# Kernel tuning notes

Measured on AMD Instinct MI355X. Metric: run time of the kernel, lower is better.

The kernel has to match this reference:

```python
import jax, jax.numpy as jnp
import numpy as np

DIM = 48
D_STATE = 16
D_CONV = 4
EXPAND = 2
D_INNER = DIM * EXPAND          # 96
DT_RANK = (DIM + 15) // 16      # 3
EPS = 1e-5


def _interp2x_align_corners(x, axis):
    """Linear 2x upsample along one axis with align_corners=True."""
    n = x.shape[axis]
    out = 2 * n
    pos = jnp.arange(out, dtype=jnp.float32) * (n - 1) / (out - 1)
    lo = jnp.floor(pos).astype(jnp.int32)
    hi = jnp.minimum(lo + 1, n - 1)
    w = (pos - lo.astype(jnp.float32)).astype(x.dtype)
    shape = [1] * x.ndim
    shape[axis] = out
    w = w.reshape(shape)
    return jnp.take(x, lo, axis=axis) * (1 - w) + jnp.take(x, hi, axis=axis) * w


def _upsample_trilinear2x(x):
    for axis in (2, 3, 4):
        x = _interp2x_align_corners(x, axis)
    return x


def _conv3d(x, w, b, pad):
    y = jax.lax.conv_general_dilated(
        x, w, window_strides=(1, 1, 1), padding=[(pad, pad)] * 3,
        dimension_numbers=('NCDHW', 'OIDHW', 'NCDHW'))
    return y + b[None, :, None, None, None]


def _instance_norm(x):
    m = x.mean(axis=(2, 3, 4), keepdims=True)
    v = x.var(axis=(2, 3, 4), keepdims=True)  # biased var, as PyTorch InstanceNorm3d
    return (x - m) / jnp.sqrt(v + EPS)


def _mamba(u, in_proj_w, conv1d_w, conv1d_b, x_proj_w, dt_proj_w, dt_proj_b,
           A_log, D_param, out_proj_w):
    # u: (B, L, d_model)
    Bsz, L, _ = u.shape
    xz = jnp.einsum('bld,ed->ble', u, in_proj_w)        # (B, L, 2*Di)
    xi, z = jnp.split(xz, 2, axis=-1)                   # each (B, L, Di)
    # depthwise causal conv1d (pad left d_conv-1, crop to L == mamba's slice)
    xpad = jnp.pad(xi.transpose(0, 2, 1), ((0, 0), (0, 0), (D_CONV - 1, 0)))
    xc = jax.lax.conv_general_dilated(
        xpad, conv1d_w, window_strides=(1,), padding=[(0, 0)],
        dimension_numbers=('NCH', 'OIH', 'NCH'), feature_group_count=D_INNER)
    xs = jax.nn.silu((xc + conv1d_b[None, :, None]).transpose(0, 2, 1))  # (B, L, Di)

    dbc = jnp.einsum('bld,ed->ble', xs, x_proj_w)       # (B, L, dt_rank+2*N)
    dt, Bm, Cm = jnp.split(dbc, [DT_RANK, DT_RANK + D_STATE], axis=-1)
    delta = jax.nn.softplus(jnp.einsum('blr,dr->bld', dt, dt_proj_w) + dt_proj_b)

    A = -jnp.exp(A_log)                                  # (Di, N)
    dA = jnp.exp(jnp.einsum('bld,dn->bldn', delta, A))   # (B, L, Di, N)
    dBx = jnp.einsum('bld,bln->bldn', delta * xs, Bm)    # (B, L, Di, N)

    def step(h, inp):
        dA_t, dBx_t, C_t = inp                           # (B,Di,N),(B,Di,N),(B,N)
        h = dA_t * h + dBx_t
        y = jnp.einsum('bdn,bn->bd', h, C_t)
        return h, y

    h0 = jnp.zeros((Bsz, D_INNER, D_STATE), xs.dtype)
    _, ys = jax.lax.scan(step, h0,
                         (dA.transpose(1, 0, 2, 3), dBx.transpose(1, 0, 2, 3),
                          Cm.transpose(1, 0, 2)))
    y = ys.transpose(1, 0, 2) + D_param[None, None, :] * xs
    y = y * jax.nn.silu(z)
    return jnp.einsum('bld,ed->ble', y, out_proj_w)      # (B, L, d_model)


def setup_inputs() -> dict:
    key = jax.random.key(0)
    ks = jax.random.split(key, 16)
    s = 0.05
    f32 = jnp.float32
    inp = {
        'x': jax.random.normal(ks[0], (2, DIM, 12, 12, 12), f32),
        'Hx': jax.random.normal(ks[1], (2, DIM * 2, 24, 24, 24), f32),
        'W1': jax.random.normal(ks[2], (DIM, DIM * 3, 1, 1, 1), f32) * s,
        'b1': jax.random.normal(ks[3], (DIM,), f32) * s,
        'W2': jax.random.normal(ks[4], (DIM, DIM, 3, 3, 3), f32) * s,
        'b2': jax.random.normal(ks[5], (DIM,), f32) * s,
        'W3': jax.random.normal(ks[6], (DIM, DIM, 1, 1, 1), f32) * s,
        'b3': jax.random.normal(ks[7], (DIM,), f32) * s,
        'in_proj_w': jax.random.normal(ks[8], (2 * D_INNER, DIM), f32) * s,
        'conv1d_w': jax.random.normal(ks[9], (D_INNER, 1, D_CONV), f32) * s,
        'conv1d_b': jax.random.normal(ks[10], (D_INNER,), f32) * s,
        'x_proj_w': jax.random.normal(ks[11], (DT_RANK + 2 * D_STATE, D_INNER), f32) * s,
        'dt_proj_w': jax.random.normal(ks[12], (D_INNER, DT_RANK), f32) * s,
        'dt_proj_b': jax.random.normal(ks[13], (D_INNER,), f32) * 0.1,
        'A_log': jnp.log(jnp.tile(jnp.arange(1, D_STATE + 1, dtype=f32)[None, :],
                                  (D_INNER, 1))),
        'D_param': jnp.ones((D_INNER,), f32),
        'out_proj_w': jax.random.normal(ks[14], (DIM, D_INNER), f32) * s,
    }
    return inp


def reference(x, Hx, W1, b1, W2, b2, W3, b3, in_proj_w, conv1d_w, conv1d_b,
              x_proj_w, dt_proj_w, dt_proj_b, A_log, D_param, out_proj_w):
    up = _upsample_trilinear2x(x)                         # (B, dim, 2H, 2W, 2T)
    h = jnp.concatenate([up, Hx], axis=1)                 # (B, 3*dim, ...)
    h = _conv3d(h, W1, b1, 0)
    h = _conv3d(h, W2, b2, 1)
    h = _conv3d(h, W3, b3, 0)
    Lx = jax.nn.selu(_instance_norm(h))
    B, C, H, W, T = Lx.shape
    u = Lx.reshape(B, C, H * W * T).transpose(0, 2, 1)    # (B, L, C)
    ym = _mamba(u, in_proj_w, conv1d_w, conv1d_b, x_proj_w, dt_proj_w,
                dt_proj_b, A_log, D_param, out_proj_w)
    out = ym.transpose(0, 2, 1).reshape(B, C, H, W, T) + Lx
    return out
```

## Files before the change

### kernel.cpp

```cpp
#include <hip/hip_runtime.h>
#include <math.h>

#define NB 2
#define NCH 48
#define P 13824
#define DI 96
#define NSTATE 16
#define L 13824
#define CHUNK 128
#define NCK 108
#define TL 64

__device__ __forceinline__ float siluf(float x) { return x / (1.f + __expf(-x)); }
__device__ __forceinline__ float softplusf(float x) {
    return x > 0.f ? x + log1pf(expf(-x)) : log1pf(expf(x));
}

__global__ __launch_bounds__(256) void k_wtrans(const float* __restrict__ W2,
    const float* __restrict__ W1, const float* __restrict__ W3,
    const float* __restrict__ Wop, float* __restrict__ Wt, float* __restrict__ W1t,
    float* __restrict__ W3t, float* __restrict__ Wopt)
{
    int i = blockIdx.x * 256 + threadIdx.x;
    if (i < 62208) {
        int o = i / (48 * 27); int r = i % (48 * 27); int c = r / 27; int tap = r % 27;
        int og = o / 12, oi = o % 12;
        Wt[(((og * 27 + tap) * 48 + c) * 12) + oi] = W2[i];
    } else if (i < 62208 + 6912) {
        int j = i - 62208; int o = j / 144, c = j % 144;
        W1t[c * 48 + o] = W1[j];
    } else if (i < 62208 + 6912 + 2304) {
        int j = i - 62208 - 6912; int o = j / 48, c = j % 48;
        W3t[c * 48 + o] = W3[j];
    } else if (i < 62208 + 6912 + 2304 + 4608) {
        int j = i - 62208 - 6912 - 2304; int o = j / 96, q = j % 96;
        Wopt[q * 48 + o] = Wop[j];
    }
}

__global__ __launch_bounds__(128) void k_conv1(const float* __restrict__ x,
    const float* __restrict__ Hx, const float* __restrict__ W1t,
    const float* __restrict__ b1, float* __restrict__ h1)
{
    int t = blockIdx.x * 128 + threadIdx.x;
    int oh = blockIdx.y * 24;
    int b = t / P, p = t % P;
    int zi = p / 576, yi = (p / 24) % 24, xi_ = p % 24;
    float fpos; int z0, z1, y0, y1, x0, x1; float wz, wy, wx;
    fpos = (float)(zi * 11) / 23.0f; z0 = (int)floorf(fpos); wz = fpos - z0; z1 = min(z0 + 1, 11);
    fpos = (float)(yi * 11) / 23.0f; y0 = (int)floorf(fpos); wy = fpos - y0; y1 = min(y0 + 1, 11);
    fpos = (float)(xi_ * 11) / 23.0f; x0 = (int)floorf(fpos); wx = fpos - x0; x1 = min(x0 + 1, 11);
    int o000 = (z0*12+y0)*12+x0, o001 = (z0*12+y0)*12+x1;
    int o010 = (z0*12+y1)*12+x0, o011 = (z0*12+y1)*12+x1;
    int o100 = (z1*12+y0)*12+x0, o101 = (z1*12+y0)*12+x1;
    int o110 = (z1*12+y1)*12+x0, o111 = (z1*12+y1)*12+x1;
    float uz = 1.f - wz, uy = 1.f - wy, ux = 1.f - wx;
    float w000 = uz*uy*ux, w001 = uz*uy*wx, w010 = uz*wy*ux, w011 = uz*wy*wx;
    float w100 = wz*uy*ux, w101 = wz*uy*wx, w110 = wz*wy*ux, w111 = wz*wy*wx;

    float acc[24];
#pragma unroll
    for (int o = 0; o < 24; ++o) acc[o] = b1[oh + o];
    const float* xb = x + (size_t)b * 48 * 1728;
    for (int c0 = 0; c0 < 48; c0 += 4) {
        float a[4][8];
#pragma unroll
        for (int j = 0; j < 4; ++j) {
            const float* xc = xb + (c0 + j) * 1728;
            a[j][0] = xc[o000]; a[j][1] = xc[o001]; a[j][2] = xc[o010]; a[j][3] = xc[o011];
            a[j][4] = xc[o100]; a[j][5] = xc[o101]; a[j][6] = xc[o110]; a[j][7] = xc[o111];
        }
#pragma unroll
        for (int j = 0; j < 4; ++j) {
            float v = a[j][0]*w000 + a[j][1]*w001 + a[j][2]*w010 + a[j][3]*w011
                    + a[j][4]*w100 + a[j][5]*w101 + a[j][6]*w110 + a[j][7]*w111;
            const float* wr = W1t + (c0 + j) * 48 + oh;
#pragma unroll
            for (int o = 0; o < 24; ++o) acc[o] = fmaf(wr[o], v, acc[o]);
        }
    }
    const float* hb = Hx + (size_t)b * 96 * P + p;
    for (int c0 = 0; c0 < 96; c0 += 8) {
        float v[8];
#pragma unroll
        for (int j = 0; j < 8; ++j) v[j] = hb[(size_t)(c0 + j) * P];
#pragma unroll
        for (int j = 0; j < 8; ++j) {
            const float* wr = W1t + (48 + c0 + j) * 48 + oh;
#pragma unroll
            for (int o = 0; o < 24; ++o) acc[o] = fmaf(wr[o], v[j], acc[o]);
        }
    }
    float* out = h1 + (size_t)b * 48 * P + p;
#pragma unroll
    for (int o = 0; o < 24; ++o) out[(size_t)(oh+o) * P] = acc[o];
}

__global__ __launch_bounds__(512) void k_conv23(const float* __restrict__ h1,
    const float* __restrict__ Wt, const float* __restrict__ b2,
    const float* __restrict__ W3t, const float* __restrict__ b3,
    float* __restrict__ h3)
{
    __shared__ float tile[216 * 52];
    int blk = blockIdx.x;
    int b = blk / 216; int r = blk % 216;
    int tz = r / 36, ty = (r / 6) % 6, tx = r % 6;
    int z0 = tz*4 - 1, y0 = ty*4 - 1, x0 = tx*4 - 1;
    for (int i = threadIdx.x; i < 48 * 216; i += 512) {
        int c = i / 216; int q = i % 216;
        int lz = q / 36, ly = (q / 6) % 6, lx = q % 6;
        int gz = z0 + lz, gy = y0 + ly, gx = x0 + lx;
        float v = 0.f;
        if ((unsigned)gz < 24u && (unsigned)gy < 24u && (unsigned)gx < 24u)
            v = h1[((size_t)(b*48 + c)) * P + (gz*24 + gy)*24 + gx];
        tile[q*52 + c] = v;
    }
    __syncthreads();
    int lp = threadIdx.x & 63;
    int w  = __builtin_amdgcn_readfirstlane((int)(threadIdx.x >> 6));
    int og = w & 3, cc = w >> 2;
    int lz = lp >> 4, ly = (lp >> 2) & 3, lx = lp & 3;
    float acc[12];
#pragma unroll
    for (int i = 0; i < 12; ++i) acc[i] = cc ? 0.f : b2[og*12 + i];
#pragma unroll
    for (int dz = 0; dz < 3; ++dz)
#pragma unroll
    for (int dy = 0; dy < 3; ++dy)
#pragma unroll
    for (int dx = 0; dx < 3; ++dx) {
        int pos = (lz+dz)*36 + (ly+dy)*6 + (lx+dx);
        const float* tp = tile + pos*52 + cc*24;
        int tap = (dz*3 + dy)*3 + dx;
        const float* wt = Wt + (((size_t)og*27 + tap)*48 + cc*24)*12;
#pragma unroll
        for (int cq = 0; cq < 6; ++cq) {
            float4 v4 = *(const float4*)(tp + cq*4);
            const float* wq = wt + cq*48;
#pragma unroll
            for (int i = 0; i < 12; ++i) {
                acc[i] = fmaf(wq[i],      v4.x, acc[i]);
                acc[i] = fmaf(wq[12 + i], v4.y, acc[i]);
                acc[i] = fmaf(wq[24 + i], v4.z, acc[i]);
                acc[i] = fmaf(wq[36 + i], v4.w, acc[i]);
            }
        }
    }
    __syncthreads();
    if (cc == 1) {
        float* ex = tile + og * 768;
#pragma unroll
        for (int i = 0; i < 12; ++i) ex[i*64 + lp] = acc[i];
    }
    __syncthreads();
    if (cc == 0) {
        const float* ex = tile + og * 768;
        float* ht = tile + 3072;
#pragma unroll
        for (int i = 0; i < 12; ++i)
            ht[(og*12 + i)*64 + lp] = acc[i] + ex[i*64 + lp];
    }
    __syncthreads();
    const float* ht = tile + 3072;
    int oc0 = w * 6;
    float acc3[6];
#pragma unroll
    for (int j = 0; j < 6; ++j) acc3[j] = b3[oc0 + j];
    for (int c = 0; c < 48; ++c) {
        float v = ht[c*64 + lp];
        const float* wr = W3t + c*48 + oc0;
#pragma unroll
        for (int j = 0; j < 6; ++j) acc3[j] = fmaf(wr[j], v, acc3[j]);
    }
    int gz = tz*4 + lz, gy = ty*4 + ly, gx = tx*4 + lx;
    size_t pp = (size_t)(gz*24 + gy)*24 + gx;
#pragma unroll
    for (int j = 0; j < 6; ++j)
        h3[((size_t)(b*48) + oc0 + j) * P + pp] = acc3[j];
}

__global__ __launch_bounds__(256) void k_instnorm(float* __restrict__ h3)
{
    int bc = blockIdx.x;
    float4* src = (float4*)(h3 + (size_t)bc * P);
    float s = 0.f, s2 = 0.f;
    for (int i = threadIdx.x; i < 3456; i += 256) {
        float4 v = src[i];
        s  += v.x + v.y + v.z + v.w;
        s2 += v.x*v.x + v.y*v.y + v.z*v.z + v.w*v.w;
    }
    __shared__ float rs[4], rs2[4], mv[2];
    for (int off = 32; off; off >>= 1) { s += __shfl_down(s, off); s2 += __shfl_down(s2, off); }
    int wid = threadIdx.x >> 6;
    if ((threadIdx.x & 63) == 0) { rs[wid] = s; rs2[wid] = s2; }
    __syncthreads();
    if (threadIdx.x == 0) {
        s = rs[0] + rs[1] + rs[2] + rs[3];
        s2 = rs2[0] + rs2[1] + rs2[2] + rs2[3];
        float m = s / (float)P;
        float var = s2 / (float)P - m * m;
        mv[0] = m; mv[1] = rsqrtf(var + 1e-5f);
    }
    __syncthreads();
    float m = mv[0], istd = mv[1];
    const float kS = 1.0507009873554805f, kA = 1.6732632423543772f;
    for (int i = threadIdx.x; i < 3456; i += 256) {
        float4 v = src[i];
        float a0 = (v.x - m) * istd, a1 = (v.y - m) * istd;
        float a2 = (v.z - m) * istd, a3 = (v.w - m) * istd;
        v.x = a0 > 0.f ? kS * a0 : kS * kA * expm1f(a0);
        v.y = a1 > 0.f ? kS * a1 : kS * kA * expm1f(a1);
        v.z = a2 > 0.f ? kS * a2 : kS * kA * expm1f(a2);
        v.w = a3 > 0.f ? kS * a3 : kS * kA * expm1f(a3);
        src[i] = v;
    }
}

__global__ __launch_bounds__(192) void k_inproj(const float* __restrict__ Lx,
    const float* __restrict__ Wip, float* __restrict__ xi, float* __restrict__ z)
{
    int b = blockIdx.x / 432; int l0 = (blockIdx.x % 432) * 32;
    int e = threadIdx.x;
    float w[48];
#pragma unroll
    for (int c = 0; c < 48; ++c) w[c] = Wip[e*48 + c];
    float acc[32];
#pragma unroll
    for (int ll = 0; ll < 32; ++ll) acc[ll] = 0.f;
    const float* ub = Lx + (size_t)b * 48 * P + l0;
#pragma unroll 2
    for (int c = 0; c < 48; ++c) {
        const float* ur = ub + (size_t)c * P;
#pragma unroll
        for (int ll = 0; ll < 32; ++ll) acc[ll] = fmaf(w[c], ur[ll], acc[ll]);
    }
    float* dst = (e < 96) ? (xi + ((size_t)b * L + l0) * 96 + e)
                          : (z  + ((size_t)b * L + l0) * 96 + (e - 96));
#pragma unroll
    for (int ll = 0; ll < 32; ++ll) dst[(size_t)ll * 96] = acc[ll];
}

__global__ __launch_bounds__(256) void k_fxproj(const float* __restrict__ xi,
    const float* __restrict__ cw, const float* __restrict__ cb,
    const float* __restrict__ Wxp, const float* __restrict__ Wdt,
    const float* __restrict__ bdt, float* __restrict__ xs,
    float* __restrict__ delta, float* __restrict__ Bm, float* __restrict__ Cm)
{
    __shared__ float xs_t[TL][100];
    __shared__ float wx_t[35][100];
    __shared__ float wd_t[96][4];
    __shared__ float dt_t[TL][4];
    int blk = blockIdx.x;
    int b = blk / 216; int l0 = (blk % 216) * TL;
    int tid = threadIdx.x;

    for (int i = tid; i < 35 * 96; i += 256) wx_t[i / 96][i % 96] = Wxp[i];
    for (int i = tid; i < 96 * 3; i += 256) wd_t[i / 3][i % 3] = Wdt[i];
    for (int i = tid; i < 96; i += 256) wd_t[i][3] = bdt[i];

    int row = tid >> 2;
    int d0 = (tid & 3) * 24;
    int l = l0 + row;
    size_t t_glob = (size_t)b * L + l;
    const float* xib = xi + (size_t)b * L * 96;
    float* xsg = xs + t_glob * 96 + d0;
    int ls0 = l - 3;
#pragma unroll
    for (int jq = 0; jq < 6; ++jq) {
        int d = d0 + jq * 4;
        float4 t0 = *(const float4*)(cw + 4 * (d + 0));
        float4 t1 = *(const float4*)(cw + 4 * (d + 1));
        float4 t2 = *(const float4*)(cw + 4 * (d + 2));
        float4 t3 = *(const float4*)(cw + 4 * (d + 3));
        float4 acc = *(const float4*)(cb + d);
        float4 q0 = {0.f,0.f,0.f,0.f}, q1 = q0, q2 = q0;
        if (ls0 + 0 >= 0) q0 = *(const float4*)(xib + (size_t)(ls0 + 0) * 96 + d);
        if (ls0 + 1 >= 0) q1 = *(const float4*)(xib + (size_t)(ls0 + 1) * 96 + d);
        if (ls0 + 2 >= 0) q2 = *(const float4*)(xib + (size_t)(ls0 + 2) * 96 + d);
        float4 q3 = *(const float4*)(xib + (size_t)(ls0 + 3) * 96 + d);
        acc.x += t0.x*q0.x + t0.y*q1.x + t0.z*q2.x + t0.w*q3.x;
        acc.y += t1.x*q0.y + t1.y*q1.y + t1.z*q2.y + t1.w*q3.y;
        acc.z += t2.x*q0.z + t2.y*q1.z + t2.z*q2.z + t2.w*q3.z;
        acc.w += t3.x*q0.w + t3.y*q1.w + t3.z*q2.w + t3.w*q3.w;
        acc.x = siluf(acc.x); acc.y = siluf(acc.y);
        acc.z = siluf(acc.z); acc.w = siluf(acc.w);
        *(float4*)(&xs_t[row][d0 + jq * 4]) = acc;
        *(float4*)(xsg + jq * 4) = acc;
    }
    __syncthreads();

    int cq = tid & 3;
    float acc9[9];
#pragma unroll
    for (int k = 0; k < 9; ++k) acc9[k] = 0.f;
    const float* xrow = &xs_t[row][0];
#pragma unroll 4
    for (int j = 0; j < 24; ++j) {
        float4 xv = *(const float4*)(xrow + 4 * j);
#pragma unroll
        for (int k = 0; k < 9; ++k) {
            if (k < 8 || cq < 3) {
                int e = cq + 4 * k;
                float4 wv = *(const float4*)(&wx_t[e][4 * j]);
                acc9[k] = fmaf(wv.x, xv.x, fmaf(wv.y, xv.y,
                          fmaf(wv.z, xv.z, fmaf(wv.w, xv.w, acc9[k]))));
            }
        }
    }
#pragma unroll
    for (int k = 0; k < 9; ++k) {
        if (k < 8 || cq < 3) {
            int e = cq + 4 * k;
            if (e < 3)       dt_t[row][e] = acc9[k];
            else if (e < 19) Bm[t_glob * 16 + (e - 3)]  = acc9[k];
            else             Cm[t_glob * 16 + (e - 19)] = acc9[k];
        }
    }
    __syncthreads();

    float dt0 = dt_t[row][0], dt1 = dt_t[row][1], dt2 = dt_t[row][2];
    float* dl = delta + t_glob * 96 + d0;
#pragma unroll
    for (int jq = 0; jq < 6; ++jq) {
        float4 o;
        {
            float4 wv = *(const float4*)(&wd_t[d0 + jq*4 + 0][0]);
            o.x = softplusf(fmaf(wv.x, dt0, fmaf(wv.y, dt1, fmaf(wv.z, dt2, wv.w))));
        }
        {
            float4 wv = *(const float4*)(&wd_t[d0 + jq*4 + 1][0]);
            o.y = softplusf(fmaf(wv.x, dt0, fmaf(wv.y, dt1, fmaf(wv.z, dt2, wv.w))));
        }
        {
            float4 wv = *(const float4*)(&wd_t[d0 + jq*4 + 2][0]);
            o.z = softplusf(fmaf(wv.x, dt0, fmaf(wv.y, dt1, fmaf(wv.z, dt2, wv.w))));
        }
        {
            float4 wv = *(const float4*)(&wd_t[d0 + jq*4 + 3][0]);
            o.w = softplusf(fmaf(wv.x, dt0, fmaf(wv.y, dt1, fmaf(wv.z, dt2, wv.w))));
        }
        *(float4*)(dl + jq * 4) = o;
    }
}

__global__ __launch_bounds__(256) void k_scan1(const float* __restrict__ delta,
    const float* __restrict__ xs, const float* __restrict__ Bm,
    const float* __restrict__ Alog, float* __restrict__ Aprod, float* __restrict__ hend)
{
    int wid = (blockIdx.x * 256 + threadIdx.x) >> 6;
    int lane = threadIdx.x & 63;
    int dg = wid % 24; int ch = (wid / 24) % NCK; int b = wid / (24 * NCK);
    int dl = lane >> 4, n = lane & 15;
    int d = dg * 4 + dl;
    float A = -__expf(Alog[d*16 + n]);
    float h = 0.f, ap = 1.f;
    int t0 = ch * CHUNK;
    const float* dp = delta + ((size_t)b * L + t0) * 96 + d;
    const float* xp = xs    + ((size_t)b * L + t0) * 96 + d;
    const float* bp = Bm    + ((size_t)b * L + t0) * 16 + n;

    float dA0, dA1, dA2, dA3, xA0, xA1, xA2, xA3, bA0, bA1, bA2, bA3;
    float dB0, dB1, dB2, dB3, xB0, xB1, xB2, xB3, bB0, bB1, bB2, bB3;
#define LD1(s, T) do { \
    d##s##0 = dp[(size_t)(T)*96];     x##s##0 = xp[(size_t)(T)*96];     b##s##0 = bp[(size_t)(T)*16]; \
    d##s##1 = dp[(size_t)((T)+1)*96]; x##s##1 = xp[(size_t)((T)+1)*96]; b##s##1 = bp[(size_t)((T)+1)*16]; \
    d##s##2 = dp[(size_t)((T)+2)*96]; x##s##2 = xp[(size_t)((T)+2)*96]; b##s##2 = bp[(size_t)((T)+2)*16]; \
    d##s##3 = dp[(size_t)((T)+3)*96]; x##s##3 = xp[(size_t)((T)+3)*96]; b##s##3 = bp[(size_t)((T)+3)*16]; \
  } while (0)
#define CMP1(s) do { \
    float e0 = __expf(d##s##0 * A); float e1 = __expf(d##s##1 * A); \
    float e2 = __expf(d##s##2 * A); float e3 = __expf(d##s##3 * A); \
    h = fmaf(e0, h, d##s##0 * x##s##0 * b##s##0); \
    h = fmaf(e1, h, d##s##1 * x##s##1 * b##s##1); \
    h = fmaf(e2, h, d##s##2 * x##s##2 * b##s##2); \
    h = fmaf(e3, h, d##s##3 * x##s##3 * b##s##3); \
    ap *= e0 * e1 * e2 * e3; \
  } while (0)

    LD1(A, 0);
#pragma unroll 1
    for (int t = 0; t < CHUNK; t += 8) {
        LD1(B, t + 4);
        CMP1(A);
        if (t + 8 < CHUNK) LD1(A, t + 8);
        CMP1(B);
    }
#undef LD1
#undef CMP1
    size_t idx = (((size_t)b * NCK + ch) * 96 + d) * 16 + n;
    Aprod[idx] = ap;
    hend[idx]  = h;
}

__global__ __launch_bounds__(256) void k_scan2(const float* __restrict__ Aprod,
    const float* __restrict__ hend, float* __restrict__ hin)
{
    int t = blockIdx.x * 256 + threadIdx.x;
    int b = t / 1536; int dn = t % 1536;
    const float* ap = Aprod + (size_t)b * NCK * 1536 + dn;
    const float* he = hend  + (size_t)b * NCK * 1536 + dn;
    float* hi       = hin   + (size_t)b * NCK * 1536 + dn;
    float carry = 0.f;
    float aA0, aA1, aA2, aA3, hA0, hA1, hA2, hA3;
    float aB0, aB1, aB2, aB3, hB0, hB1, hB2, hB3;
#define LD2(s, J) do { \
    a##s##0 = ap[(size_t)(J)*1536];     h##s##0 = he[(size_t)(J)*1536]; \
    a##s##1 = ap[(size_t)((J)+1)*1536]; h##s##1 = he[(size_t)((J)+1)*1536]; \
    a##s##2 = ap[(size_t)((J)+2)*1536]; h##s##2 = he[(size_t)((J)+2)*1536]; \
    a##s##3 = ap[(size_t)((J)+3)*1536]; h##s##3 = he[(size_t)((J)+3)*1536]; \
  } while (0)
#define CMP2(s, J) do { \
    hi[(size_t)(J)*1536]     = carry; carry = fmaf(a##s##0, carry, h##s##0); \
    hi[(size_t)((J)+1)*1536] = carry; carry = fmaf(a##s##1, carry, h##s##1); \
    hi[(size_t)((J)+2)*1536] = carry; carry = fmaf(a##s##2, carry, h##s##2); \
    hi[(size_t)((J)+3)*1536] = carry; carry = fmaf(a##s##3, carry, h##s##3); \
  } while (0)
    LD2(A, 0);
#pragma unroll 1
    for (int j = 0; j < 104; j += 8) {
        LD2(B, j + 4);
        CMP2(A, j);
        if (j + 8 < NCK) LD2(A, j + 8);
        CMP2(B, j + 4);
    }
    LD2(A, 104);
    CMP2(A, 104);
#undef LD2
#undef CMP2
}

__global__ __launch_bounds__(256) void k_scan3(const float* __restrict__ delta,
    float* __restrict__ xs, const float* __restrict__ Bm, const float* __restrict__ Cm,
    const float* __restrict__ z, const float* __restrict__ Alog,
    const float* __restrict__ Dp, const float* __restrict__ hin)
{
    int wid = (blockIdx.x * 256 + threadIdx.x) >> 6;
    int lane = threadIdx.x & 63;
    int dg = wid % 24; int ch = (wid / 24) % NCK; int b = wid / (24 * NCK);
    int dl = lane >> 4, n = lane & 15;
    int d = dg * 4 + dl;
    float A = -__expf(Alog[d*16 + n]);
    float Dv = Dp[d];
    size_t cidx = (((size_t)b * NCK + ch) * 96 + d) * 16 + n;
    float h = hin[cidx];
    int t0 = ch * CHUNK;
    const float* dp = delta + ((size_t)b * L + t0) * 96 + d;
    float* xp       = xs    + ((size_t)b * L + t0) * 96 + d;
    const float* bp = Bm    + ((size_t)b * L + t0) * 16 + n;
    const float* cp = Cm    + ((size_t)b * L + t0) * 16 + n;
    const float* zp = z     + ((size_t)b * L + t0) * 96 + d;

    float dA0, dA1, dA2, dA3, xA0, xA1, xA2, xA3, bA0, bA1, bA2, bA3, cA0, cA1, cA2, cA3, zA0, zA1, zA2, zA3;
    float dB0, dB1, dB2, dB3, xB0, xB1, xB2, xB3, bB0, bB1, bB2, bB3, cB0, cB1, cB2, cB3, zB0, zB1, zB2, zB3;
#define LD3(s, T) do { \
    d##s##0 = dp[(size_t)(T)*96];     x##s##0 = xp[(size_t)(T)*96];     b##s##0 = bp[(size_t)(T)*16]; \
    c##s##0 = cp[(size_t)(T)*16];     z##s##0 = zp[(size_t)(T)*96]; \
    d##s##1 = dp[(size_t)((T)+1)*96]; x##s##1 = xp[(size_t)((T)+1)*96]; b##s##1 = bp[(size_t)((T)+1)*16]; \
    c##s##1 = cp[(size_t)((T)+1)*16]; z##s##1 = zp[(size_t)((T)+1)*96]; \
    d##s##2 = dp[(size_t)((T)+2)*96]; x##s##2 = xp[(size_t)((T)+2)*96]; b##s##2 = bp[(size_t)((T)+2)*16]; \
    c##s##2 = cp[(size_t)((T)+2)*16]; z##s##2 = zp[(size_t)((T)+2)*96]; \
    d##s##3 = dp[(size_t)((T)+3)*96]; x##s##3 = xp[(size_t)((T)+3)*96]; b##s##3 = bp[(size_t)((T)+3)*16]; \
    c##s##3 = cp[(size_t)((T)+3)*16]; z##s##3 = zp[(size_t)((T)+3)*96]; \
  } while (0)
#define STEP3(DEL, XV, BV, CV, ZV, T) do { \
    float dAv = __expf((DEL) * A); \
    h = fmaf(dAv, h, (DEL) * (XV) * (BV)); \
    float yc = h * (CV); \
    yc += __shfl_xor(yc, 8); \
    yc += __shfl_xor(yc, 4); \
    yc += __shfl_xor(yc, 2); \
    yc += __shfl_xor(yc, 1); \
    if (n == 0) xp[(size_t)(T)*96] = fmaf(Dv, (XV), yc) * siluf(ZV); \
  } while (0)
#define CMP3(s, T) do { \
    STEP3(d##s##0, x##s##0, b##s##0, c##s##0, z##s##0, (T)); \
    STEP3(d##s##1, x##s##1, b##s##1, c##s##1, z##s##1, (T)+1); \
    STEP3(d##s##2, x##s##2, b##s##2, c##s##2, z##s##2, (T)+2); \
    STEP3(d##s##3, x##s##3, b##s##3, c##s##3, z##s##3, (T)+3); \
  } while (0)

    LD3(A, 0);
#pragma unroll 1
    for (int t = 0; t < CHUNK; t += 8) {
        LD3(B, t + 4);
        CMP3(A, t);
        if (t + 8 < CHUNK) LD3(A, t + 8);
        CMP3(B, t + 4);
    }
#undef LD3
#undef STEP3
#undef CMP3
}

__global__ __launch_bounds__(128) void k_outproj(const float* __restrict__ y,
    const float* __restrict__ Wopt, const float* __restrict__ Lx, float* __restrict__ out)
{
    int t = blockIdx.x * 128 + threadIdx.x;
    int oh = blockIdx.y * 24;
    int b = t / P, p = t % P;
    const float* yr = y + (size_t)t * 96;
    float acc[24];
#pragma unroll
    for (int o = 0; o < 24; ++o) acc[o] = 0.f;
#pragma unroll
    for (int i = 0; i < 24; ++i) {
        float4 v4 = ((const float4*)yr)[i];
        const float* w0 = Wopt + (i*4) * 48 + oh;
        const float* w1 = Wopt + (i*4 + 1) * 48 + oh;
        const float* w2 = Wopt + (i*4 + 2) * 48 + oh;
        const float* w3 = Wopt + (i*4 + 3) * 48 + oh;
#pragma unroll
        for (int o = 0; o < 24; ++o) {
            acc[o] = fmaf(w0[o], v4.x, acc[o]);
            acc[o] = fmaf(w1[o], v4.y, acc[o]);
            acc[o] = fmaf(w2[o], v4.z, acc[o]);
            acc[o] = fmaf(w3[o], v4.w, acc[o]);
        }
    }
    const float* lx = Lx + (size_t)b * 48 * P + p;
    float* op = out + (size_t)b * 48 * P + p;
#pragma unroll
    for (int o = 0; o < 24; ++o) op[(size_t)(oh+o) * P] = acc[o] + lx[(size_t)(oh+o) * P];
}

extern "C" void kernel_launch(void* const* d_in, const int* in_sizes, int n_in,
                              void* d_out, int out_size, void* d_ws, size_t ws_size,
                              hipStream_t stream) {
    const float* x        = (const float*)d_in[0];
    const float* Hx       = (const float*)d_in[1];
    const float* W1       = (const float*)d_in[2];
    const float* b1       = (const float*)d_in[3];
    const float* W2       = (const float*)d_in[4];
    const float* b2       = (const float*)d_in[5];
    const float* W3       = (const float*)d_in[6];
    const float* b3       = (const float*)d_in[7];
    const float* in_proj  = (const float*)d_in[8];
    const float* conv1d_w = (const float*)d_in[9];
    const float* conv1d_b = (const float*)d_in[10];
    const float* x_proj   = (const float*)d_in[11];
    const float* dt_proj  = (const float*)d_in[12];
    const float* dt_bias  = (const float*)d_in[13];
    const float* A_log    = (const float*)d_in[14];
    const float* D_param  = (const float*)d_in[15];
    const float* out_proj = (const float*)d_in[16];
    float* out = (float*)d_out;

    float* ws = (float*)d_ws;
    const size_t SZ_BCP = (size_t)NB * 48 * P;
    const size_t SZ_BLD = (size_t)NB * L * 96;
    const size_t SZ_BLN = (size_t)NB * L * 16;
    const size_t SZ_CK  = (size_t)NB * NCK * 1536;
    float* bufA  = ws;
    float* bufB  = bufA + SZ_BCP;
    float* bufC  = bufB + SZ_BCP;
    float* xib   = bufC + SZ_BCP;
    float* zb    = xib  + SZ_BLD;
    float* xsb   = zb   + SZ_BLD;
    float* Bmb   = xsb  + SZ_BLD;
    float* Cmb   = Bmb  + SZ_BLN;
    float* Apr   = Cmb  + SZ_BLN;
    float* hendb = Apr  + SZ_CK;
    float* hinb  = hendb+ SZ_CK;
    float* stats = hinb + SZ_CK;
    float* Wtb   = stats + 192;
    float* W1tb  = Wtb + 62208;
    float* W3tb  = W1tb + 6912;
    float* Woptb = W3tb + 2304;
    float* deltab = bufA;

    k_wtrans<<<297, 256, 0, stream>>>(W2, W1, W3, out_proj, Wtb, W1tb, W3tb, Woptb);
    k_conv1<<<dim3(216, 2), 128, 0, stream>>>(x, Hx, W1tb, b1, bufA);
    k_conv23<<<NB * 216, 512, 0, stream>>>(bufA, Wtb, b2, W3tb, b3, bufC);
    k_instnorm<<<NB * 48, 256, 0, stream>>>(bufC);
    k_inproj<<<NB * 432, 192, 0, stream>>>(bufC, in_proj, xib, zb);
    k_fxproj<<<NB * 216, 256, 0, stream>>>(xib, conv1d_w, conv1d_b, x_proj, dt_proj,
                                           dt_bias, xsb, deltab, Bmb, Cmb);
    k_scan1<<<(NB * NCK * 24) / 4, 256, 0, stream>>>(deltab, xsb, Bmb, A_log, Apr, hendb);
    k_scan2<<<12, 256, 0, stream>>>(Apr, hendb, hinb);
    k_scan3<<<(NB * NCK * 24) / 4, 256, 0, stream>>>(deltab, xsb, Bmb, Cmb, zb, A_log,
                                                     D_param, hinb);
    k_outproj<<<dim3(216, 2), 128, 0, stream>>>(xsb, Woptb, bufC, out);
}
```

Before: 274.9 us.

## Map one thread per channel with all 16 states in registers for scans

The chunked selective scan kernels now give each thread a whole inner channel and keep all 16 state values in registers. Each block covers one (batch, chunk) pair with 128 threads, 96 of them active. This removes the four-step cross-lane shuffle reduction over states and the redundant loads of delta, x and z across 16 lanes, and B and C rows are read with vector loads. In exchange there are far fewer threads (216 blocks of 128), a quarter of each block idles on the padded lanes, and register pressure rises, so latency hiding on the GPU may suffer.

```diff
diff --git a/kernel.cpp b/kernel.cpp
--- a/kernel.cpp
+++ b/kernel.cpp
@@ -343,53 +343,65 @@
     }
 }
 
-__global__ __launch_bounds__(256) void k_scan1(const float* __restrict__ delta,
+__global__ __launch_bounds__(128) void k_scan1(const float* __restrict__ delta,
     const float* __restrict__ xs, const float* __restrict__ Bm,
     const float* __restrict__ Alog, float* __restrict__ Aprod, float* __restrict__ hend)
 {
-    int wid = (blockIdx.x * 256 + threadIdx.x) >> 6;
-    int lane = threadIdx.x & 63;
-    int dg = wid % 24; int ch = (wid / 24) % NCK; int b = wid / (24 * NCK);
-    int dl = lane >> 4, n = lane & 15;
-    int d = dg * 4 + dl;
-    float A = -__expf(Alog[d*16 + n]);
-    float h = 0.f, ap = 1.f;
+    int blk = blockIdx.x;
+    int b = blk / NCK, ch = blk % NCK;
+    int d = threadIdx.x;
+    int dc = d < 96 ? d : 95;
     int t0 = ch * CHUNK;
-    const float* dp = delta + ((size_t)b * L + t0) * 96 + d;
-    const float* xp = xs    + ((size_t)b * L + t0) * 96 + d;
-    const float* bp = Bm    + ((size_t)b * L + t0) * 16 + n;
-
-    float dA0, dA1, dA2, dA3, xA0, xA1, xA2, xA3, bA0, bA1, bA2, bA3;
-    float dB0, dB1, dB2, dB3, xB0, xB1, xB2, xB3, bB0, bB1, bB2, bB3;
-#define LD1(s, T) do { \
-    d##s##0 = dp[(size_t)(T)*96];     x##s##0 = xp[(size_t)(T)*96];     b##s##0 = bp[(size_t)(T)*16]; \
-    d##s##1 = dp[(size_t)((T)+1)*96]; x##s##1 = xp[(size_t)((T)+1)*96]; b##s##1 = bp[(size_t)((T)+1)*16]; \
-    d##s##2 = dp[(size_t)((T)+2)*96]; x##s##2 = xp[(size_t)((T)+2)*96]; b##s##2 = bp[(size_t)((T)+2)*16]; \
-    d##s##3 = dp[(size_t)((T)+3)*96]; x##s##3 = xp[(size_t)((T)+3)*96]; b##s##3 = bp[(size_t)((T)+3)*16]; \
+    const float* dp = delta + ((size_t)b * L + t0) * 96 + dc;
+    const float* xp = xs    + ((size_t)b * L + t0) * 96 + dc;
+    const float* bp = Bm    + ((size_t)b * L + t0) * 16;
+    float A[16], h[16], ap[16];
+    {
+        const float* ar = Alog + dc * 16;
+#pragma unroll
+        for (int n = 0; n < 16; ++n) { A[n] = -__expf(ar[n]); h[n] = 0.f; ap[n] = 1.f; }
+    }
+    float delA, xvA, delB, xvB;
+    float bmA[16], bmB[16];
+#define LDP1(s, T) do { \
+    del##s = dp[(size_t)(T)*96]; xv##s = xp[(size_t)(T)*96]; \
+    float4 q0 = *(const float4*)(bp + (size_t)(T)*16); \
+    float4 q1 = *(const float4*)(bp + (size_t)(T)*16 + 4); \
+    float4 q2 = *(const float4*)(bp + (size_t)(T)*16 + 8); \
+    float4 q3 = *(const float4*)(bp + (size_t)(T)*16 + 12); \
+    bm##s[0]=q0.x; bm##s[1]=q0.y; bm##s[2]=q0.z; bm##s[3]=q0.w; \
+    bm##s[4]=q1.x; bm##s[5]=q1.y; bm##s[6]=q1.z; bm##s[7]=q1.w; \
+    bm##s[8]=q2.x; bm##s[9]=q2.y; bm##s[10]=q2.z; bm##s[11]=q2.w; \
+    bm##s[12]=q3.x; bm##s[13]=q3.y; bm##s[14]=q3.z; bm##s[15]=q3.w; \
   } while (0)
-#define CMP1(s) do { \
-    float e0 = __expf(d##s##0 * A); float e1 = __expf(d##s##1 * A); \
-    float e2 = __expf(d##s##2 * A); float e3 = __expf(d##s##3 * A); \
-    h = fmaf(e0, h, d##s##0 * x##s##0 * b##s##0); \
-    h = fmaf(e1, h, d##s##1 * x##s##1 * b##s##1); \
-    h = fmaf(e2, h, d##s##2 * x##s##2 * b##s##2); \
-    h = fmaf(e3, h, d##s##3 * x##s##3 * b##s##3); \
-    ap *= e0 * e1 * e2 * e3; \
+#define CMPP1(s) do { \
+    float dx = del##s * xv##s; \
+    _Pragma("unroll") \
+    for (int n = 0; n < 16; ++n) { \
+        float e = __expf(del##s * A[n]); \
+        h[n] = fmaf(e, h[n], dx * bm##s[n]); \
+        ap[n] *= e; \
+    } \
   } while (0)
-
-    LD1(A, 0);
+    LDP1(A, 0);
 #pragma unroll 1
-    for (int t = 0; t < CHUNK; t += 8) {
-        LD1(B, t + 4);
-        CMP1(A);
-        if (t + 8 < CHUNK) LD1(A, t + 8);
-        CMP1(B);
-    }
-#undef LD1
-#undef CMP1
-    size_t idx = (((size_t)b * NCK + ch) * 96 + d) * 16 + n;
-    Aprod[idx] = ap;
-    hend[idx]  = h;
+    for (int t = 0; t < CHUNK; t += 2) {
+        if (t + 1 < CHUNK) LDP1(B, t + 1);
+        CMPP1(A);
+        if (t + 2 < CHUNK) LDP1(A, t + 2);
+        CMPP1(B);
+    }
+#undef LDP1
+#undef CMPP1
+    if (d < 96) {
+        float* apo = Aprod + (((size_t)b * NCK + ch) * 96 + d) * 16;
+        float* heo = hend  + (((size_t)b * NCK + ch) * 96 + d) * 16;
+#pragma unroll
+        for (int n = 0; n < 16; n += 4) {
+            *(float4*)(apo + n) = make_float4(ap[n], ap[n+1], ap[n+2], ap[n+3]);
+            *(float4*)(heo + n) = make_float4(h[n], h[n+1], h[n+2], h[n+3]);
+        }
+    }
 }
 
 __global__ __launch_bounds__(256) void k_scan2(const float* __restrict__ Aprod,
@@ -429,67 +441,71 @@
 #undef CMP2
 }
 
-__global__ __launch_bounds__(256) void k_scan3(const float* __restrict__ delta,
+__global__ __launch_bounds__(128) void k_scan3(const float* __restrict__ delta,
     float* __restrict__ xs, const float* __restrict__ Bm, const float* __restrict__ Cm,
     const float* __restrict__ z, const float* __restrict__ Alog,
     const float* __restrict__ Dp, const float* __restrict__ hin)
 {
-    int wid = (blockIdx.x * 256 + threadIdx.x) >> 6;
-    int lane = threadIdx.x & 63;
-    int dg = wid % 24; int ch = (wid / 24) % NCK; int b = wid / (24 * NCK);
-    int dl = lane >> 4, n = lane & 15;
-    int d = dg * 4 + dl;
-    float A = -__expf(Alog[d*16 + n]);
-    float Dv = Dp[d];
-    size_t cidx = (((size_t)b * NCK + ch) * 96 + d) * 16 + n;
-    float h = hin[cidx];
+    int blk = blockIdx.x;
+    int b = blk / NCK, ch = blk % NCK;
+    int d = threadIdx.x;
+    int dc = d < 96 ? d : 95;
     int t0 = ch * CHUNK;
-    const float* dp = delta + ((size_t)b * L + t0) * 96 + d;
-    float* xp       = xs    + ((size_t)b * L + t0) * 96 + d;
-    const float* bp = Bm    + ((size_t)b * L + t0) * 16 + n;
-    const float* cp = Cm    + ((size_t)b * L + t0) * 16 + n;
-    const float* zp = z     + ((size_t)b * L + t0) * 96 + d;
-
-    float dA0, dA1, dA2, dA3, xA0, xA1, xA2, xA3, bA0, bA1, bA2, bA3, cA0, cA1, cA2, cA3, zA0, zA1, zA2, zA3;
-    float dB0, dB1, dB2, dB3, xB0, xB1, xB2, xB3, bB0, bB1, bB2, bB3, cB0, cB1, cB2, cB3, zB0, zB1, zB2, zB3;
-#define LD3(s, T) do { \
-    d##s##0 = dp[(size_t)(T)*96];     x##s##0 = xp[(size_t)(T)*96];     b##s##0 = bp[(size_t)(T)*16]; \
-    c##s##0 = cp[(size_t)(T)*16];     z##s##0 = zp[(size_t)(T)*96]; \
-    d##s##1 = dp[(size_t)((T)+1)*96]; x##s##1 = xp[(size_t)((T)+1)*96]; b##s##1 = bp[(size_t)((T)+1)*16]; \
-    c##s##1 = cp[(size_t)((T)+1)*16]; z##s##1 = zp[(size_t)((T)+1)*96]; \
-    d##s##2 = dp[(size_t)((T)+2)*96]; x##s##2 = xp[(size_t)((T)+2)*96]; b##s##2 = bp[(size_t)((T)+2)*16]; \
-    c##s##2 = cp[(size_t)((T)+2)*16]; z##s##2 = zp[(size_t)((T)+2)*96]; \
-    d##s##3 = dp[(size_t)((T)+3)*96]; x##s##3 = xp[(size_t)((T)+3)*96]; b##s##3 = bp[(size_t)((T)+3)*16]; \
-    c##s##3 = cp[(size_t)((T)+3)*16]; z##s##3 = zp[(size_t)((T)+3)*96]; \
+    const float* dp = delta + ((size_t)b * L + t0) * 96 + dc;
+    float* xp       = xs    + ((size_t)b * L + t0) * 96 + dc;
+    const float* zp = z     + ((size_t)b * L + t0) * 96 + dc;
+    const float* bp = Bm    + ((size_t)b * L + t0) * 16;
+    const float* cp = Cm    + ((size_t)b * L + t0) * 16;
+    float Dv = Dp[dc];
+    float A[16], h[16];
+    {
+        const float* ar = Alog + dc * 16;
+        const float* hr = hin + (((size_t)b * NCK + ch) * 96 + dc) * 16;
+#pragma unroll
+        for (int n = 0; n < 16; ++n) { A[n] = -__expf(ar[n]); h[n] = hr[n]; }
+    }
+    float delA, xvA, zvA, delB, xvB, zvB;
+    float bmA[16], bmB[16], cmA[16], cmB[16];
+#define LDP3(s, T) do { \
+    del##s = dp[(size_t)(T)*96]; xv##s = xp[(size_t)(T)*96]; zv##s = zp[(size_t)(T)*96]; \
+    float4 q0 = *(const float4*)(bp + (size_t)(T)*16); \
+    float4 q1 = *(const float4*)(bp + (size_t)(T)*16 + 4); \
+    float4 q2 = *(const float4*)(bp + (size_t)(T)*16 + 8); \
+    float4 q3 = *(const float4*)(bp + (size_t)(T)*16 + 12); \
+    bm##s[0]=q0.x; bm##s[1]=q0.y; bm##s[2]=q0.z; bm##s[3]=q0.w; \
+    bm##s[4]=q1.x; bm##s[5]=q1.y; bm##s[6]=q1.z; bm##s[7]=q1.w; \
+    bm##s[8]=q2.x; bm##s[9]=q2.y; bm##s[10]=q2.z; bm##s[11]=q2.w; \
+    bm##s[12]=q3.x; bm##s[13]=q3.y; bm##s[14]=q3.z; bm##s[15]=q3.w; \
+    q0 = *(const float4*)(cp + (size_t)(T)*16); \
+    q1 = *(const float4*)(cp + (size_t)(T)*16 + 4); \
+    q2 = *(const float4*)(cp + (size_t)(T)*16 + 8); \
+    q3 = *(const float4*)(cp + (size_t)(T)*16 + 12); \
+    cm##s[0]=q0.x; cm##s[1]=q0.y; cm##s[2]=q0.z; cm##s[3]=q0.w; \
+    cm##s[4]=q1.x; cm##s[5]=q1.y; cm##s[6]=q1.z; cm##s[7]=q1.w; \
+    cm##s[8]=q2.x; cm##s[9]=q2.y; cm##s[10]=q2.z; cm##s[11]=q2.w; \
+    cm##s[12]=q3.x; cm##s[13]=q3.y; cm##s[14]=q3.z; cm##s[15]=q3.w; \
   } while (0)
-#define STEP3(DEL, XV, BV, CV, ZV, T) do { \
-    float dAv = __expf((DEL) * A); \
-    h = fmaf(dAv, h, (DEL) * (XV) * (BV)); \
-    float yc = h * (CV); \
-    yc += __shfl_xor(yc, 8); \
-    yc += __shfl_xor(yc, 4); \
-    yc += __shfl_xor(yc, 2); \
-    yc += __shfl_xor(yc, 1); \
-    if (n == 0) xp[(size_t)(T)*96] = fmaf(Dv, (XV), yc) * siluf(ZV); \
+#define CMPP3(s, T) do { \
+    float dx = del##s * xv##s; \
+    float y = 0.f; \
+    _Pragma("unroll") \
+    for (int n = 0; n < 16; ++n) { \
+        float e = __expf(del##s * A[n]); \
+        h[n] = fmaf(e, h[n], dx * bm##s[n]); \
+        y = fmaf(h[n], cm##s[n], y); \
+    } \
+    if (d < 96) xp[(size_t)(T)*96] = fmaf(Dv, xv##s, y) * siluf(zv##s); \
   } while (0)
-#define CMP3(s, T) do { \
-    STEP3(d##s##0, x##s##0, b##s##0, c##s##0, z##s##0, (T)); \
-    STEP3(d##s##1, x##s##1, b##s##1, c##s##1, z##s##1, (T)+1); \
-    STEP3(d##s##2, x##s##2, b##s##2, c##s##2, z##s##2, (T)+2); \
-    STEP3(d##s##3, x##s##3, b##s##3, c##s##3, z##s##3, (T)+3); \
-  } while (0)
-
-    LD3(A, 0);
+    LDP3(A, 0);
 #pragma unroll 1
-    for (int t = 0; t < CHUNK; t += 8) {
-        LD3(B, t + 4);
-        CMP3(A, t);
-        if (t + 8 < CHUNK) LD3(A, t + 8);
-        CMP3(B, t + 4);
-    }
-#undef LD3
-#undef STEP3
-#undef CMP3
+    for (int t = 0; t < CHUNK; t += 2) {
+        if (t + 1 < CHUNK) LDP3(B, t + 1);
+        CMPP3(A, t);
+        if (t + 2 < CHUNK) LDP3(A, t + 2);
+        CMPP3(B, t + 1);
+    }
+#undef LDP3
+#undef CMPP3
 }
 
 __global__ __launch_bounds__(128) void k_outproj(const float* __restrict__ y,
@@ -575,9 +591,9 @@
     k_inproj<<<NB * 432, 192, 0, stream>>>(bufC, in_proj, xib, zb);
     k_fxproj<<<NB * 216, 256, 0, stream>>>(xib, conv1d_w, conv1d_b, x_proj, dt_proj,
                                            dt_bias, xsb, deltab, Bmb, Cmb);
-    k_scan1<<<(NB * NCK * 24) / 4, 256, 0, stream>>>(deltab, xsb, Bmb, A_log, Apr, hendb);
+    k_scan1<<<NB * NCK, 128, 0, stream>>>(deltab, xsb, Bmb, A_log, Apr, hendb);
     k_scan2<<<12, 256, 0, stream>>>(Apr, hendb, hinb);
-    k_scan3<<<(NB * NCK * 24) / 4, 256, 0, stream>>>(deltab, xsb, Bmb, Cmb, zb, A_log,
-                                                     D_param, hinb);
+    k_scan3<<<NB * NCK, 128, 0, stream>>>(deltab, xsb, Bmb, Cmb, zb, A_log,
+                                          D_param, hinb);
     k_outproj<<<dim3(216, 2), 128, 0, stream>>>(xsb, Woptb, bufC, out);
 }
```

Result: slower. 308.8 us (+12.3%).
